# Kernel tuning notes

Hardware: AMD Instinct MI355X
Metric: run time of the kernel (lower is better)

The kernel has to match this reference:

```python
import jax, jax.numpy as jnp
import numpy as np

B, S, H = 2, 256, 768
LR = 0.01
EPS = 1e-5  # torch LayerNorm default


def setup_inputs() -> dict:
    key = jax.random.key(0)
    ks = jax.random.split(key, 6)
    f = jnp.float32
    return {
        "x": jax.random.normal(ks[0], (B, S, H), f),
        "W_init": jax.random.normal(ks[1], (H, H), f) * 0.02,
        "b_init": jnp.zeros((H,), f),
        "gate_w": jax.random.normal(ks[2], (4 * H, H), f) * 0.02,
        "gate_b": jnp.zeros((4 * H,), f),
        "up_w": jax.random.normal(ks[3], (4 * H, H), f) * 0.02,
        "up_b": jnp.zeros((4 * H,), f),
        "down_w": jax.random.normal(ks[4], (H, 4 * H), f) * 0.02,
        "down_b": jnp.zeros((H,), f),
        "norm_w": jnp.ones((H,), f),
        "norm_b": jnp.zeros((H,), f),
    }


def _layernorm(x, w, b):
    mu = jnp.mean(x, axis=-1, keepdims=True)
    var = jnp.var(x, axis=-1, keepdims=True)
    return (x - mu) * jax.lax.rsqrt(var + EPS) * w + b


def reference(x, W_init, b_init, gate_w, gate_b, up_w, up_b,
              down_w, down_b, norm_w, norm_b):
    # x: [B, S, H]. Sequential TTT fast-weight recurrence, vectorized over batch,
    # scanned over time (equivalent to the per-token Python loop in torch).
    Bn, Sn, Hn = x.shape
    xs = jnp.swapaxes(x, 0, 1)                                   # [S, B, H]
    x_next = jnp.concatenate([xs[1:], jnp.zeros_like(xs[:1])], 0)  # target x[t+1]
    # lr per step; the update is skipped at the last token (t == S-1)
    lr = jnp.concatenate([jnp.full((Sn - 1,), LR, x.dtype),
                          jnp.zeros((1,), x.dtype)])

    W0 = jnp.broadcast_to(W_init, (Bn, Hn, Hn))
    b0 = jnp.broadcast_to(b_init, (Bn, Hn))

    def step(carry, inp):
        W, b = carry
        xt, xn, lr_t = inp
        pred = jnp.einsum('bij,bj->bi', W, xt) + b               # fast-weight matvec
        gated = jax.nn.sigmoid(pred @ gate_w.T + gate_b) * (pred @ up_w.T + up_b)
        out = _layernorm(gated @ down_w.T + down_b + pred, norm_w, norm_b)
        diff = pred - xn                                         # prediction error
        W = W - lr_t * diff[:, :, None] * xt[:, None, :]         # rank-1 update
        b = b - lr_t * diff
        return (W, b), out

    _, ys = jax.lax.scan(step, (W0, b0), (xs, x_next, lr))       # ys: [S, B, H]
    return jnp.swapaxes(ys, 0, 1)
```

## Files before the change

kernel.cpp:

```cpp
#include <hip/hip_runtime.h>
#include <hip/hip_bf16.h>

#define H   768
#define H4  3072
#define S   256
#define BB  2
#define M   (BB * S)
#define LRC 0.01f
#define C   64
#define NC  (S / C)

typedef __attribute__((ext_vector_type(8))) short bf16x8;
typedef __attribute__((ext_vector_type(4))) float f32x4;

__device__ inline short bfbits(float f) {
    __hip_bfloat16 h = __float2bfloat16(f);
    return *reinterpret_cast<short*>(&h);
}

__global__ __launch_bounds__(256) void k_stage(
    const float* __restrict__ x,  const float* __restrict__ W0,
    const float* __restrict__ gw, const float* __restrict__ uw,
    const float* __restrict__ dw,
    short* __restrict__ Xhi, short* __restrict__ Xlo,
    short* __restrict__ Whi, short* __restrict__ Wlo,
    short* __restrict__ gw2, short* __restrict__ uw2, short* __restrict__ dw2)
{
    const long gid = (long)blockIdx.x * 256 + threadIdx.x;
    const float* src; short* hp; short* lp = nullptr; long base;
    if (gid < 98304)        { src = x;  hp = Xhi; lp = Xlo; base = 0; }
    else if (gid < 245760)  { src = W0; hp = Whi; lp = Wlo; base = 98304; }
    else if (gid < 835584)  { src = gw; hp = gw2; base = 245760; }
    else if (gid < 1425408) { src = uw; hp = uw2; base = 835584; }
    else                    { src = dw; hp = dw2; base = 1425408; }
    const long i = (gid - base) * 4;
    const float4 v = *(const float4*)(src + i);
    const float vf[4] = {v.x, v.y, v.z, v.w};
    short h4[4], l4[4];
#pragma unroll
    for (int j = 0; j < 4; ++j) {
        h4[j] = bfbits(vf[j]);
        __hip_bfloat16 hb = *reinterpret_cast<__hip_bfloat16*>(&h4[j]);
        l4[j] = bfbits(vf[j] - __bfloat162float(hb));
    }
    *(uint2*)(hp + i) = *(uint2*)h4;
    if (lp) *(uint2*)(lp + i) = *(uint2*)l4;
}

__global__ __launch_bounds__(256) void k_gram_base(
    const short* __restrict__ Xhi, const short* __restrict__ Xlo,
    const short* __restrict__ Whi, const short* __restrict__ Wlo,
    const float* __restrict__ b0,
    float* __restrict__ g, float* __restrict__ base0)
{
    const int wid = threadIdx.x >> 6, lane = threadIdx.x & 63;
    const int r16 = lane & 15, quad = lane >> 4;
    const int id = blockIdx.x;

    f32x4 acc[4];
#pragma unroll
    for (int i = 0; i < 4; ++i) acc[i] = (f32x4){0, 0, 0, 0};

    if (id < 32) {
        const int bx = id & 3, by = (id >> 2) & 3, b = id >> 4;
        const int m0 = by * 64, n0 = bx * 64 + wid * 16;
        const short* XH = Xhi + b * S * H;
        const short* XL = Xlo + b * S * H;
        for (int k0 = 0; k0 < H; k0 += 32) {
            const int k = k0 + quad * 8;
            const bf16x8 bh = *(const bf16x8*)(XH + (n0 + r16) * H + k);
            const bf16x8 bl = *(const bf16x8*)(XL + (n0 + r16) * H + k);
#pragma unroll
            for (int i = 0; i < 4; ++i) {
                const bf16x8 ah = *(const bf16x8*)(XH + (m0 + i * 16 + r16) * H + k);
                const bf16x8 al = *(const bf16x8*)(XL + (m0 + i * 16 + r16) * H + k);
                acc[i] = __builtin_amdgcn_mfma_f32_16x16x32_bf16(ah, bh, acc[i], 0, 0, 0);
                acc[i] = __builtin_amdgcn_mfma_f32_16x16x32_bf16(ah, bl, acc[i], 0, 0, 0);
                acc[i] = __builtin_amdgcn_mfma_f32_16x16x32_bf16(al, bh, acc[i], 0, 0, 0);
            }
        }
        const int col = n0 + r16;
#pragma unroll
        for (int i = 0; i < 4; ++i)
#pragma unroll
            for (int r = 0; r < 4; ++r) {
                const int row = m0 + i * 16 + quad * 4 + r;
                g[(b * S + row) * S + col] = acc[i][r] + 1.f;
            }
    } else {
        const int id2 = id - 32;
        const int m0 = (id2 / 12) * 64, n0 = (id2 % 12) * 64 + wid * 16;
        for (int k0 = 0; k0 < H; k0 += 32) {
            const int k = k0 + quad * 8;
            const bf16x8 bh = *(const bf16x8*)(Whi + (n0 + r16) * H + k);
            const bf16x8 bl = *(const bf16x8*)(Wlo + (n0 + r16) * H + k);
#pragma unroll
            for (int i = 0; i < 4; ++i) {
                const bf16x8 ah = *(const bf16x8*)(Xhi + (m0 + i * 16 + r16) * H + k);
                const bf16x8 al = *(const bf16x8*)(Xlo + (m0 + i * 16 + r16) * H + k);
                acc[i] = __builtin_amdgcn_mfma_f32_16x16x32_bf16(ah, bh, acc[i], 0, 0, 0);
                acc[i] = __builtin_amdgcn_mfma_f32_16x16x32_bf16(ah, bl, acc[i], 0, 0, 0);
                acc[i] = __builtin_amdgcn_mfma_f32_16x16x32_bf16(al, bh, acc[i], 0, 0, 0);
            }
        }
        const int col = n0 + r16;
        const float bv = b0[col];
#pragma unroll
        for (int i = 0; i < 4; ++i)
#pragma unroll
            for (int r = 0; r < 4; ++r) {
                const int row = m0 + i * 16 + quad * 4 + r;
                base0[row * H + col] = acc[i][r] + bv;
            }
    }
}

__global__ __launch_bounds__(256) void k_inv(
    const float* __restrict__ g, float* __restrict__ U)
{
    __shared__ float Gi[C * 65];
    const int tid = threadIdx.x;
    const int w = tid >> 6, lane = tid & 63;
    const int b = blockIdx.x >> 2, c = blockIdx.x & 3;
    const int t0 = c * C;

#pragma unroll
    for (int j = 0; j < 16; ++j) {
        const int idx = tid + 256 * j;
        const int row = idx >> 6, col = idx & 63;
        Gi[row * 65 + col] = g[(long)(b * S + t0 + row) * S + t0 + col];
    }
    __syncthreads();

    const int j0 = w * 16;
    float R[16];
#pragma unroll
    for (int i = 0; i < 16; ++i) R[i] = (lane == j0 + i) ? 1.f : 0.f;

    for (int s = 0; s < C - 1; ++s) {
        const float Gv = Gi[s * 65 + lane];
        const float mlt = (lane > s) ? LRC : 0.f;
#pragma unroll
        for (int i = 0; i < 16; ++i) {
            const float dsb = __shfl(R[i], s, 64);
            R[i] -= mlt * Gv * dsb;
        }
    }
    float* Ub = U + (long)(b * NC + c) * C * C;
#pragma unroll
    for (int i = 0; i < 16; ++i)
        Ub[lane * C + j0 + i] = R[i];
}

__global__ __launch_bounds__(256) void k_recur5(
    const float* __restrict__ x,
    const float* __restrict__ base0,
    const float* __restrict__ g,
    const float* __restrict__ U,
    float* __restrict__ pred_f,
    __hip_bfloat16* __restrict__ pred_h)
{
    __shared__ float tB[64 * 17];
    __shared__ float tX[64 * 17];
    __shared__ float Dl[256 * 17];
    __shared__ float Us[64 * 65];
    __shared__ float Gslab[192 * 64];
    const int tid = threadIdx.x;
    const int w = tid >> 6, lane = tid & 63;
    const int b = blockIdx.x / 48, hb = blockIdx.x % 48;
    const int h0 = hb * 16;
    const int ho = w * 4;
    const int ct = tid >> 2;
    const int cq = (tid & 3) * 4;

    for (int c = 0; c < NC; ++c) {
        const int t0 = c * C;
        __syncthreads();
        {
            const int gm = b * S + t0 + ct;
            const float4 bv = *(const float4*)(base0 + gm * H + h0 + cq);
            float4 xv = {0.f, 0.f, 0.f, 0.f};
            if (t0 + ct + 1 < S)
                xv = *(const float4*)(x + (gm + 1) * H + h0 + cq);
            tB[ct * 17 + cq + 0] = bv.x - xv.x;
            tB[ct * 17 + cq + 1] = bv.y - xv.y;
            tB[ct * 17 + cq + 2] = bv.z - xv.z;
            tB[ct * 17 + cq + 3] = bv.w - xv.w;
            tX[ct * 17 + cq + 0] = xv.x;
            tX[ct * 17 + cq + 1] = xv.y;
            tX[ct * 17 + cq + 2] = xv.z;
            tX[ct * 17 + cq + 3] = xv.w;
            const float* Ub = U + (long)(b * NC + c) * C * C;
#pragma unroll
            for (int j = 0; j < 16; ++j) {
                const int idx = tid + 256 * j;
                const int row = idx >> 6, col = idx & 63;
                Us[row * 65 + col] = Ub[row * C + col];
            }
            const float* gb = g + (long)(b * S) * S + t0;
            for (int i = tid; i < t0 * 64; i += 256) {
                const int row = i >> 6, col = i & 63;
                Gslab[i] = gb[(long)row * S + col];
            }
        }
        __syncthreads();
        float R[4], Xn[4];
#pragma unroll
        for (int h = 0; h < 4; ++h) {
            R[h]  = tB[lane * 17 + ho + h];
            Xn[h] = tX[lane * 17 + ho + h];
        }
#pragma unroll 4
        for (int cs = 0; cs < t0; ++cs) {
            const float Gv = Gslab[cs * 64 + lane];
            const float* dr = &Dl[cs * 17 + ho];
            R[0] -= LRC * Gv * dr[0];
            R[1] -= LRC * Gv * dr[1];
            R[2] -= LRC * Gv * dr[2];
            R[3] -= LRC * Gv * dr[3];
        }
        float D[4] = {0.f, 0.f, 0.f, 0.f};
#pragma unroll 8
        for (int s = 0; s < C; ++s) {
            const float Gv = Us[lane * 65 + s];
#pragma unroll
            for (int h = 0; h < 4; ++h) {
                const float dsb = __shfl(R[h], s, 64);
                D[h] += Gv * dsb;
            }
        }
#pragma unroll
        for (int h = 0; h < 4; ++h) Dl[(t0 + lane) * 17 + ho + h] = D[h];
        __syncthreads();
#pragma unroll
        for (int h = 0; h < 4; ++h) tB[lane * 17 + ho + h] = D[h] + Xn[h];
        __syncthreads();
        {
            const int gm = b * S + t0 + ct;
            float4 pv;
            pv.x = tB[ct * 17 + cq + 0];
            pv.y = tB[ct * 17 + cq + 1];
            pv.z = tB[ct * 17 + cq + 2];
            pv.w = tB[ct * 17 + cq + 3];
            *(float4*)(pred_f + gm * H + h0 + cq) = pv;
            short p4[4];
            p4[0] = bfbits(pv.x); p4[1] = bfbits(pv.y);
            p4[2] = bfbits(pv.z); p4[3] = bfbits(pv.w);
            *(uint2*)((short*)pred_h + gm * H + h0 + cq) = *(uint2*)p4;
        }
    }
}

#define RS 40
__global__ __launch_bounds__(256) void k_gateup3(
    const __hip_bfloat16* __restrict__ predh,
    const short* __restrict__ gwp, const float* __restrict__ gb,
    const short* __restrict__ uwp, const float* __restrict__ ub,
    __hip_bfloat16* __restrict__ hid)
{
    __shared__ int4 smv[1600];
    short* sm = (short*)smv;
    short* sA = sm;
    short* sG = sm + 64 * RS;
    short* sU = sm + (64 + 128) * RS;

    const int tid = threadIdx.x;
    const int wid = tid >> 6, lane = tid & 63;
    const int r16 = lane & 15, quad = lane >> 4;
    const int wm = wid & 1, wn = wid >> 1;
    const int n0 = blockIdx.x * 128;
    const int m0 = blockIdx.y * 64;

    const int srow = tid >> 2;
    const int sch  = (tid & 3) * 8;
    const short* A = (const short*)predh;

    f32x4 ag[2][4], au[2][4];
#pragma unroll
    for (int i = 0; i < 2; ++i)
#pragma unroll
        for (int j = 0; j < 4; ++j) { ag[i][j] = (f32x4){0,0,0,0}; au[i][j] = (f32x4){0,0,0,0}; }

    int4 rA, rG0, rG1, rU0, rU1;
    {
        const int k = sch;
        rA  = *(const int4*)(A   + (m0 + srow) * H + k);
        rG0 = *(const int4*)(gwp + (n0 + srow) * H + k);
        rG1 = *(const int4*)(gwp + (n0 + 64 + srow) * H + k);
        rU0 = *(const int4*)(uwp + (n0 + srow) * H + k);
        rU1 = *(const int4*)(uwp + (n0 + 64 + srow) * H + k);
    }
    for (int it = 0; it < 24; ++it) {
        *(int4*)(sA + srow * RS + sch)        = rA;
        *(int4*)(sG + srow * RS + sch)        = rG0;
        *(int4*)(sG + (64 + srow) * RS + sch) = rG1;
        *(int4*)(sU + srow * RS + sch)        = rU0;
        *(int4*)(sU + (64 + srow) * RS + sch) = rU1;
        __syncthreads();
        if (it < 23) {
            const int k = (it + 1) * 32 + sch;
            rA  = *(const int4*)(A   + (m0 + srow) * H + k);
            rG0 = *(const int4*)(gwp + (n0 + srow) * H + k);
            rG1 = *(const int4*)(gwp + (n0 + 64 + srow) * H + k);
            rU0 = *(const int4*)(uwp + (n0 + srow) * H + k);
            rU1 = *(const int4*)(uwp + (n0 + 64 + srow) * H + k);
        }
        bf16x8 aF[2], gF[4], uF[4];
#pragma unroll
        for (int i = 0; i < 2; ++i)
            aF[i] = *(const bf16x8*)(sA + (wm * 32 + i * 16 + r16) * RS + quad * 8);
#pragma unroll
        for (int j = 0; j < 4; ++j) {
            gF[j] = *(const bf16x8*)(sG + (wn * 64 + j * 16 + r16) * RS + quad * 8);
            uF[j] = *(const bf16x8*)(sU + (wn * 64 + j * 16 + r16) * RS + quad * 8);
        }
#pragma unroll
        for (int i = 0; i < 2; ++i)
#pragma unroll
            for (int j = 0; j < 4; ++j) {
                ag[i][j] = __builtin_amdgcn_mfma_f32_16x16x32_bf16(aF[i], gF[j], ag[i][j], 0, 0, 0);
                au[i][j] = __builtin_amdgcn_mfma_f32_16x16x32_bf16(aF[i], uF[j], au[i][j], 0, 0, 0);
            }
        __syncthreads();
    }
#pragma unroll
    for (int j = 0; j < 4; ++j) {
        const int ocol = n0 + wn * 64 + j * 16 + r16;
        const float gbv = gb[ocol], ubv = ub[ocol];
#pragma unroll
        for (int i = 0; i < 2; ++i)
#pragma unroll
            for (int r = 0; r < 4; ++r) {
                const int orow = m0 + wm * 32 + i * 16 + quad * 4 + r;
                const float gg = ag[i][j][r] + gbv;
                const float u  = au[i][j][r] + ubv;
                const float sg = 1.f / (1.f + __expf(-gg));
                hid[orow * H4 + ocol] = __float2bfloat16(sg * u);
            }
    }
}

__device__ inline bf16x8 ldb16(const void* p, long off) {
    return *(const bf16x8*)((const short*)p + off);
}
__global__ __launch_bounds__(256) void k_down2b(
    const __hip_bfloat16* __restrict__ hid,
    const short* __restrict__ dwp, const float* __restrict__ db,
    const float* __restrict__ predf, float* __restrict__ dout)
{
    const int wid = threadIdx.x >> 6, lane = threadIdx.x & 63;
    const int r16 = lane & 15, quad = lane >> 4;
    const int m0 = blockIdx.y * 32;
    const int n0 = blockIdx.x * 64 + wid * 16;

    f32x4 ac[2];
    ac[0] = (f32x4){0,0,0,0}; ac[1] = (f32x4){0,0,0,0};
    const short* A = (const short*)hid;
    const long brow = (long)(n0 + r16) * H4;

    for (int k0 = 0; k0 < H4; k0 += 32) {
        const int k = k0 + quad * 8;
        const bf16x8 bd = ldb16(dwp, brow + k);
#pragma unroll
        for (int i = 0; i < 2; ++i) {
            const bf16x8 af = *(const bf16x8*)(A + (m0 + i * 16 + r16) * H4 + k);
            ac[i] = __builtin_amdgcn_mfma_f32_16x16x32_bf16(af, bd, ac[i], 0, 0, 0);
        }
    }
    const int ocol = n0 + r16;
    const float dbv = db[ocol];
#pragma unroll
    for (int i = 0; i < 2; ++i)
#pragma unroll
        for (int r = 0; r < 4; ++r) {
            const int orow = m0 + i * 16 + quad * 4 + r;
            dout[orow * H + ocol] = ac[i][r] + dbv + predf[orow * H + ocol];
        }
}

__device__ inline bf16x8 ldb32(const void* p, long off) {
    const float* f = (const float*)p + off;
    const float4 a = *(const float4*)f;
    const float4 b = *(const float4*)(f + 4);
    bf16x8 r;
    r[0] = bfbits(a.x); r[1] = bfbits(a.y); r[2] = bfbits(a.z); r[3] = bfbits(a.w);
    r[4] = bfbits(b.x); r[5] = bfbits(b.y); r[6] = bfbits(b.z); r[7] = bfbits(b.w);
    return r;
}

__global__ __launch_bounds__(256) void k_gateup2(
    const __hip_bfloat16* __restrict__ predh,
    const void* __restrict__ gw, const float* __restrict__ gb,
    const void* __restrict__ uw, const float* __restrict__ ub,
    __hip_bfloat16* __restrict__ hid)
{
    const int wid = threadIdx.x >> 6, lane = threadIdx.x & 63;
    const int r16 = lane & 15, quad = lane >> 4;
    const int m0 = blockIdx.y * 64;
    const int n0 = blockIdx.x * 64 + wid * 16;

    f32x4 ag[4], au[4];
#pragma unroll
    for (int i = 0; i < 4; ++i) { ag[i] = (f32x4){0,0,0,0}; au[i] = (f32x4){0,0,0,0}; }
    const short* A = (const short*)predh;
    const long brow = (long)(n0 + r16) * H;

    for (int k0 = 0; k0 < H; k0 += 32) {
        const int k = k0 + quad * 8;
        const bf16x8 bg = ldb32(gw, brow + k);
        const bf16x8 bu = ldb32(uw, brow + k);
#pragma unroll
        for (int i = 0; i < 4; ++i) {
            const bf16x8 af = *(const bf16x8*)(A + (m0 + i * 16 + r16) * H + k);
            ag[i] = __builtin_amdgcn_mfma_f32_16x16x32_bf16(af, bg, ag[i], 0, 0, 0);
            au[i] = __builtin_amdgcn_mfma_f32_16x16x32_bf16(af, bu, au[i], 0, 0, 0);
        }
    }
    const int ocol = n0 + r16;
    const float gbv = gb[ocol], ubv = ub[ocol];
#pragma unroll
    for (int i = 0; i < 4; ++i)
#pragma unroll
        for (int r = 0; r < 4; ++r) {
            const int orow = m0 + i * 16 + quad * 4 + r;
            const float gg = ag[i][r] + gbv;
            const float u = au[i][r] + ubv;
            const float sg = 1.f / (1.f + __expf(-gg));
            hid[orow * H4 + ocol] = __float2bfloat16(sg * u);
        }
}

__global__ __launch_bounds__(256) void k_down2f(
    const __hip_bfloat16* __restrict__ hid,
    const void* __restrict__ dw, const float* __restrict__ db,
    const float* __restrict__ predf, float* __restrict__ dout)
{
    const int wid = threadIdx.x >> 6, lane = threadIdx.x & 63;
    const int r16 = lane & 15, quad = lane >> 4;
    const int m0 = blockIdx.y * 32;
    const int n0 = blockIdx.x * 64 + wid * 16;

    f32x4 ac[2];
    ac[0] = (f32x4){0,0,0,0}; ac[1] = (f32x4){0,0,0,0};
    const short* A = (const short*)hid;
    const long brow = (long)(n0 + r16) * H4;

    for (int k0 = 0; k0 < H4; k0 += 32) {
        const int k = k0 + quad * 8;
        const bf16x8 bd = ldb32(dw, brow + k);
#pragma unroll
        for (int i = 0; i < 2; ++i) {
            const bf16x8 af = *(const bf16x8*)(A + (m0 + i * 16 + r16) * H4 + k);
            ac[i] = __builtin_amdgcn_mfma_f32_16x16x32_bf16(af, bd, ac[i], 0, 0, 0);
        }
    }
    const int ocol = n0 + r16;
    const float dbv = db[ocol];
#pragma unroll
    for (int i = 0; i < 2; ++i)
#pragma unroll
        for (int r = 0; r < 4; ++r) {
            const int orow = m0 + i * 16 + quad * 4 + r;
            dout[orow * H + ocol] = ac[i][r] + dbv + predf[orow * H + ocol];
        }
}

__global__ __launch_bounds__(256) void k_ln(
    const float* __restrict__ dout,
    const float* __restrict__ nw,
    const float* __restrict__ nb,
    float* __restrict__ out)
{
    const int m = blockIdx.x;
    const int tid = threadIdx.x;
    const float* rowp = dout + m * H;

    float v[3];
    float s = 0.f, s2 = 0.f;
#pragma unroll
    for (int j = 0; j < 3; ++j) {
        v[j] = rowp[tid + 256 * j];
        s += v[j];
        s2 += v[j] * v[j];
    }
#pragma unroll
    for (int off = 32; off >= 1; off >>= 1) {
        s  += __shfl_xor(s, off, 64);
        s2 += __shfl_xor(s2, off, 64);
    }
    __shared__ float rs[4], rs2[4];
    const int wid = tid >> 6, lane = tid & 63;
    if (lane == 0) { rs[wid] = s; rs2[wid] = s2; }
    __syncthreads();
    s  = rs[0] + rs[1] + rs[2] + rs[3];
    s2 = rs2[0] + rs2[1] + rs2[2] + rs2[3];
    const float mu  = s / (float)H;
    const float var = s2 / (float)H - mu * mu;
    const float inv = rsqrtf(var + 1e-5f);
#pragma unroll
    for (int j = 0; j < 3; ++j) {
        const int hh = tid + 256 * j;
        out[m * H + hh] = (v[j] - mu) * inv * nw[hh] + nb[hh];
    }
}

extern "C" void kernel_launch(void* const* d_in, const int* in_sizes, int n_in,
                              void* d_out, int out_size, void* d_ws, size_t ws_size,
                              hipStream_t stream)
{
    const float* x   = (const float*)d_in[0];
    const float* W0  = (const float*)d_in[1];
    const float* b0  = (const float*)d_in[2];
    const float* gw  = (const float*)d_in[3];
    const float* gb  = (const float*)d_in[4];
    const float* uw  = (const float*)d_in[5];
    const float* ub  = (const float*)d_in[6];
    const float* dw  = (const float*)d_in[7];
    const float* db  = (const float*)d_in[8];
    const float* nw  = (const float*)d_in[9];
    const float* nb  = (const float*)d_in[10];

    char* ws = (char*)d_ws;
    float*          pred_f = (float*)(ws);
    __hip_bfloat16* pred_h = (__hip_bfloat16*)(ws + 1572864);
    __hip_bfloat16* hid    = (__hip_bfloat16*)(ws + 2359296);
    float*          base0  = (float*)(ws + 5505024);
    float*          dout_f = (float*)(ws + 5505024);
    float*          g      = (float*)(ws + 7077888);
    short*          Xhi    = (short*)(ws + 7602176);
    short*          Xlo    = (short*)(ws + 8388608);
    short*          Whi    = (short*)(ws + 9175040);
    short*          Wlo    = (short*)(ws + 10354688);
    float*          U      = (float*)(ws + 11534336);
    const size_t WNEED = 11665408ULL + 3ULL * 4718592ULL;
    const bool wb = ws_size >= WNEED;
    short* gw2 = (short*)(ws + 11665408);
    short* uw2 = (short*)(ws + 11665408 + 4718592);
    short* dw2 = (short*)(ws + 11665408 + 2 * 4718592);

    const int ngroups = wb ? 2015232 : 245760;
    k_stage<<<dim3(ngroups / 256), 256, 0, stream>>>(
        x, W0, gw, uw, dw, Xhi, Xlo, Whi, Wlo, gw2, uw2, dw2);
    k_gram_base<<<dim3(128), 256, 0, stream>>>(Xhi, Xlo, Whi, Wlo, b0, g, base0);
    k_inv<<<dim3(BB * NC), 256, 0, stream>>>(g, U);
    k_recur5<<<dim3(96), 256, 0, stream>>>(x, base0, g, U, pred_f, pred_h);
    if (wb) {
        k_gateup3<<<dim3(H4 / 128, M / 64), 256, 0, stream>>>(pred_h, gw2, gb, uw2, ub, hid);
        k_down2b<<<dim3(H / 64, M / 32), 256, 0, stream>>>(hid, dw2, db, pred_f, dout_f);
    } else {
        k_gateup2<<<dim3(H4 / 64, M / 64), 256, 0, stream>>>(pred_h, gw, gb, uw, ub, hid);
        k_down2f<<<dim3(H / 64, M / 32), 256, 0, stream>>>(hid, dw, db, pred_f, dout_f);
    }
    k_ln<<<dim3(M), 256, 0, stream>>>(dout_f, nw, nb, (float*)d_out);
}
```

Measured before the change: 223.2 us.

## Split-K down projection, smaller gate/up tiles, LDS broadcast in recurrence

```diff
diff --git a/kernel.cpp b/kernel.cpp
--- a/kernel.cpp
+++ b/kernel.cpp
@@ -152,7 +152,7 @@
         Ub[lane * C + j0 + i] = R[i];
 }
 
-__global__ __launch_bounds__(256) void k_recur5(
+__global__ __launch_bounds__(256) void k_recur6(
     const float* __restrict__ x,
     const float* __restrict__ base0,
     const float* __restrict__ g,
@@ -160,11 +160,12 @@
     float* __restrict__ pred_f,
     __hip_bfloat16* __restrict__ pred_h)
 {
-    __shared__ float tB[64 * 17];
-    __shared__ float tX[64 * 17];
-    __shared__ float Dl[256 * 17];
-    __shared__ float Us[64 * 65];
-    __shared__ float Gslab[192 * 64];
+    __shared__ float  tB[64 * 17];
+    __shared__ float  tX[64 * 17];
+    __shared__ float4 Dl4[256 * 4];
+    __shared__ float4 Rl4[4 * 64];
+    __shared__ float  Us[64 * 65];
+    __shared__ float  Gslab[192 * 64];
     const int tid = threadIdx.x;
     const int w = tid >> 6, lane = tid & 63;
     const int b = blockIdx.x / 48, hb = blockIdx.x % 48;
@@ -213,24 +214,24 @@
 #pragma unroll 4
         for (int cs = 0; cs < t0; ++cs) {
             const float Gv = Gslab[cs * 64 + lane];
-            const float* dr = &Dl[cs * 17 + ho];
-            R[0] -= LRC * Gv * dr[0];
-            R[1] -= LRC * Gv * dr[1];
-            R[2] -= LRC * Gv * dr[2];
-            R[3] -= LRC * Gv * dr[3];
-        }
+            const float4 dr = Dl4[cs * 4 + w];
+            R[0] -= LRC * Gv * dr.x;
+            R[1] -= LRC * Gv * dr.y;
+            R[2] -= LRC * Gv * dr.z;
+            R[3] -= LRC * Gv * dr.w;
+        }
+        Rl4[w * 64 + lane] = (float4){R[0], R[1], R[2], R[3]};
         float D[4] = {0.f, 0.f, 0.f, 0.f};
 #pragma unroll 8
         for (int s = 0; s < C; ++s) {
-            const float Gv = Us[lane * 65 + s];
-#pragma unroll
-            for (int h = 0; h < 4; ++h) {
-                const float dsb = __shfl(R[h], s, 64);
-                D[h] += Gv * dsb;
-            }
-        }
-#pragma unroll
-        for (int h = 0; h < 4; ++h) Dl[(t0 + lane) * 17 + ho + h] = D[h];
+            const float4 rb = Rl4[w * 64 + s];
+            const float uv = Us[lane * 65 + s];
+            D[0] += uv * rb.x;
+            D[1] += uv * rb.y;
+            D[2] += uv * rb.z;
+            D[3] += uv * rb.w;
+        }
+        Dl4[(t0 + lane) * 4 + w] = (float4){D[0], D[1], D[2], D[3]};
         __syncthreads();
 #pragma unroll
         for (int h = 0; h < 4; ++h) tB[lane * 17 + ho + h] = D[h] + Xn[h];
@@ -252,80 +253,69 @@
 }
 
 #define RS 40
-__global__ __launch_bounds__(256) void k_gateup3(
+__global__ __launch_bounds__(256) void k_gateup4(
     const __hip_bfloat16* __restrict__ predh,
     const short* __restrict__ gwp, const float* __restrict__ gb,
     const short* __restrict__ uwp, const float* __restrict__ ub,
     __hip_bfloat16* __restrict__ hid)
 {
-    __shared__ int4 smv[1600];
+    __shared__ int4 smv[960];
     short* sm = (short*)smv;
     short* sA = sm;
     short* sG = sm + 64 * RS;
-    short* sU = sm + (64 + 128) * RS;
+    short* sU = sm + 128 * RS;
 
     const int tid = threadIdx.x;
     const int wid = tid >> 6, lane = tid & 63;
     const int r16 = lane & 15, quad = lane >> 4;
-    const int wm = wid & 1, wn = wid >> 1;
-    const int n0 = blockIdx.x * 128;
+    const int wm = wid & 1, wn = (wid >> 1) & 1;
+    const int n0 = blockIdx.x * 64;
     const int m0 = blockIdx.y * 64;
 
     const int srow = tid >> 2;
     const int sch  = (tid & 3) * 8;
     const short* A = (const short*)predh;
 
-    f32x4 ag[2][4], au[2][4];
+    f32x4 ag[2][2], au[2][2];
 #pragma unroll
     for (int i = 0; i < 2; ++i)
 #pragma unroll
-        for (int j = 0; j < 4; ++j) { ag[i][j] = (f32x4){0,0,0,0}; au[i][j] = (f32x4){0,0,0,0}; }
-
-    int4 rA, rG0, rG1, rU0, rU1;
-    {
-        const int k = sch;
-        rA  = *(const int4*)(A   + (m0 + srow) * H + k);
-        rG0 = *(const int4*)(gwp + (n0 + srow) * H + k);
-        rG1 = *(const int4*)(gwp + (n0 + 64 + srow) * H + k);
-        rU0 = *(const int4*)(uwp + (n0 + srow) * H + k);
-        rU1 = *(const int4*)(uwp + (n0 + 64 + srow) * H + k);
-    }
+        for (int j = 0; j < 2; ++j) { ag[i][j] = (f32x4){0,0,0,0}; au[i][j] = (f32x4){0,0,0,0}; }
+
+    int4 rA, rG, rU;
+    rA = *(const int4*)(A   + (m0 + srow) * H + sch);
+    rG = *(const int4*)(gwp + (n0 + srow) * H + sch);
+    rU = *(const int4*)(uwp + (n0 + srow) * H + sch);
     for (int it = 0; it < 24; ++it) {
-        *(int4*)(sA + srow * RS + sch)        = rA;
-        *(int4*)(sG + srow * RS + sch)        = rG0;
-        *(int4*)(sG + (64 + srow) * RS + sch) = rG1;
-        *(int4*)(sU + srow * RS + sch)        = rU0;
-        *(int4*)(sU + (64 + srow) * RS + sch) = rU1;
+        *(int4*)(sA + srow * RS + sch) = rA;
+        *(int4*)(sG + srow * RS + sch) = rG;
+        *(int4*)(sU + srow * RS + sch) = rU;
         __syncthreads();
         if (it < 23) {
             const int k = (it + 1) * 32 + sch;
-            rA  = *(const int4*)(A   + (m0 + srow) * H + k);
-            rG0 = *(const int4*)(gwp + (n0 + srow) * H + k);
-            rG1 = *(const int4*)(gwp + (n0 + 64 + srow) * H + k);
-            rU0 = *(const int4*)(uwp + (n0 + srow) * H + k);
-            rU1 = *(const int4*)(uwp + (n0 + 64 + srow) * H + k);
-        }
-        bf16x8 aF[2], gF[4], uF[4];
+            rA = *(const int4*)(A   + (m0 + srow) * H + k);
+            rG = *(const int4*)(gwp + (n0 + srow) * H + k);
+            rU = *(const int4*)(uwp + (n0 + srow) * H + k);
+        }
+        bf16x8 aF[2], gF[2], uF[2];
+#pragma unroll
+        for (int i = 0; i < 2; ++i) {
+            aF[i] = *(const bf16x8*)(sA + (wm * 32 + i * 16 + r16) * RS + quad * 8);
+            gF[i] = *(const bf16x8*)(sG + (wn * 32 + i * 16 + r16) * RS + quad * 8);
+            uF[i] = *(const bf16x8*)(sU + (wn * 32 + i * 16 + r16) * RS + quad * 8);
+        }
 #pragma unroll
         for (int i = 0; i < 2; ++i)
-            aF[i] = *(const bf16x8*)(sA + (wm * 32 + i * 16 + r16) * RS + quad * 8);
-#pragma unroll
-        for (int j = 0; j < 4; ++j) {
-            gF[j] = *(const bf16x8*)(sG + (wn * 64 + j * 16 + r16) * RS + quad * 8);
-            uF[j] = *(const bf16x8*)(sU + (wn * 64 + j * 16 + r16) * RS + quad * 8);
-        }
-#pragma unroll
-        for (int i = 0; i < 2; ++i)
-#pragma unroll
-            for (int j = 0; j < 4; ++j) {
+#pragma unroll
+            for (int j = 0; j < 2; ++j) {
                 ag[i][j] = __builtin_amdgcn_mfma_f32_16x16x32_bf16(aF[i], gF[j], ag[i][j], 0, 0, 0);
                 au[i][j] = __builtin_amdgcn_mfma_f32_16x16x32_bf16(aF[i], uF[j], au[i][j], 0, 0, 0);
             }
         __syncthreads();
     }
 #pragma unroll
-    for (int j = 0; j < 4; ++j) {
-        const int ocol = n0 + wn * 64 + j * 16 + r16;
+    for (int j = 0; j < 2; ++j) {
+        const int ocol = n0 + wn * 32 + j * 16 + r16;
         const float gbv = gb[ocol], ubv = ub[ocol];
 #pragma unroll
         for (int i = 0; i < 2; ++i)
@@ -343,22 +333,24 @@
 __device__ inline bf16x8 ldb16(const void* p, long off) {
     return *(const bf16x8*)((const short*)p + off);
 }
-__global__ __launch_bounds__(256) void k_down2b(
+__global__ __launch_bounds__(256) void k_down4(
     const __hip_bfloat16* __restrict__ hid,
-    const short* __restrict__ dwp, const float* __restrict__ db,
-    const float* __restrict__ predf, float* __restrict__ dout)
+    const short* __restrict__ dwp,
+    float* __restrict__ dpart)
 {
     const int wid = threadIdx.x >> 6, lane = threadIdx.x & 63;
     const int r16 = lane & 15, quad = lane >> 4;
     const int m0 = blockIdx.y * 32;
     const int n0 = blockIdx.x * 64 + wid * 16;
+    const int kz = blockIdx.z;
 
     f32x4 ac[2];
     ac[0] = (f32x4){0,0,0,0}; ac[1] = (f32x4){0,0,0,0};
     const short* A = (const short*)hid;
     const long brow = (long)(n0 + r16) * H4;
 
-    for (int k0 = 0; k0 < H4; k0 += 32) {
+    const int kbeg = kz * 768, kend = kbeg + 768;
+    for (int k0 = kbeg; k0 < kend; k0 += 32) {
         const int k = k0 + quad * 8;
         const bf16x8 bd = ldb16(dwp, brow + k);
 #pragma unroll
@@ -367,15 +359,60 @@
             ac[i] = __builtin_amdgcn_mfma_f32_16x16x32_bf16(af, bd, ac[i], 0, 0, 0);
         }
     }
+    float* dp = dpart + (long)kz * M * H;
     const int ocol = n0 + r16;
-    const float dbv = db[ocol];
 #pragma unroll
     for (int i = 0; i < 2; ++i)
 #pragma unroll
         for (int r = 0; r < 4; ++r) {
             const int orow = m0 + i * 16 + quad * 4 + r;
-            dout[orow * H + ocol] = ac[i][r] + dbv + predf[orow * H + ocol];
-        }
+            dp[orow * H + ocol] = ac[i][r];
+        }
+}
+
+__global__ __launch_bounds__(256) void k_ln2(
+    const float* __restrict__ dpart,
+    const float* __restrict__ db,
+    const float* __restrict__ predf,
+    const float* __restrict__ nw,
+    const float* __restrict__ nb,
+    float* __restrict__ out)
+{
+    const int m = blockIdx.x;
+    const int tid = threadIdx.x;
+
+    float v[3];
+    float s = 0.f, s2 = 0.f;
+#pragma unroll
+    for (int j = 0; j < 3; ++j) {
+        const int hh = tid + 256 * j;
+        const long o = (long)m * H + hh;
+        float t = dpart[o] + dpart[o + (long)M * H]
+                + dpart[o + 2L * M * H] + dpart[o + 3L * M * H]
+                + db[hh] + predf[o];
+        v[j] = t;
+        s += t;
+        s2 += t * t;
+    }
+#pragma unroll
+    for (int off = 32; off >= 1; off >>= 1) {
+        s  += __shfl_xor(s, off, 64);
+        s2 += __shfl_xor(s2, off, 64);
+    }
+    __shared__ float rs[4], rs2[4];
+    const int wid = tid >> 6, lane = tid & 63;
+    if (lane == 0) { rs[wid] = s; rs2[wid] = s2; }
+    __syncthreads();
+    s  = rs[0] + rs[1] + rs[2] + rs[3];
+    s2 = rs2[0] + rs2[1] + rs2[2] + rs2[3];
+    const float mu  = s / (float)H;
+    const float var = s2 / (float)H - mu * mu;
+    const float inv = rsqrtf(var + 1e-5f);
+#pragma unroll
+    for (int j = 0; j < 3; ++j) {
+        const int hh = tid + 256 * j;
+        out[m * H + hh] = (v[j] - mu) * inv * nw[hh] + nb[hh];
+    }
 }
 
 __device__ inline bf16x8 ldb32(const void* p, long off) {
@@ -465,7 +502,7 @@
         }
 }
 
-__global__ __launch_bounds__(256) void k_ln(
+__global__ __launch_bounds__(256) void k_ln1(
     const float* __restrict__ dout,
     const float* __restrict__ nw,
     const float* __restrict__ nb,
@@ -532,24 +569,26 @@
     short*          Whi    = (short*)(ws + 9175040);
     short*          Wlo    = (short*)(ws + 10354688);
     float*          U      = (float*)(ws + 11534336);
-    const size_t WNEED = 11665408ULL + 3ULL * 4718592ULL;
-    const bool wb = ws_size >= WNEED;
     short* gw2 = (short*)(ws + 11665408);
     short* uw2 = (short*)(ws + 11665408 + 4718592);
     short* dw2 = (short*)(ws + 11665408 + 2 * 4718592);
+    float* dpart = (float*)(ws + 25821184);
+    const size_t WNEED = 25821184ULL + 6291456ULL;
+    const bool wb = ws_size >= WNEED;
 
     const int ngroups = wb ? 2015232 : 245760;
     k_stage<<<dim3(ngroups / 256), 256, 0, stream>>>(
         x, W0, gw, uw, dw, Xhi, Xlo, Whi, Wlo, gw2, uw2, dw2);
     k_gram_base<<<dim3(128), 256, 0, stream>>>(Xhi, Xlo, Whi, Wlo, b0, g, base0);
     k_inv<<<dim3(BB * NC), 256, 0, stream>>>(g, U);
-    k_recur5<<<dim3(96), 256, 0, stream>>>(x, base0, g, U, pred_f, pred_h);
+    k_recur6<<<dim3(96), 256, 0, stream>>>(x, base0, g, U, pred_f, pred_h);
     if (wb) {
-        k_gateup3<<<dim3(H4 / 128, M / 64), 256, 0, stream>>>(pred_h, gw2, gb, uw2, ub, hid);
-        k_down2b<<<dim3(H / 64, M / 32), 256, 0, stream>>>(hid, dw2, db, pred_f, dout_f);
+        k_gateup4<<<dim3(H4 / 64, M / 64), 256, 0, stream>>>(pred_h, gw2, gb, uw2, ub, hid);
+        k_down4<<<dim3(H / 64, M / 32, 4), 256, 0, stream>>>(hid, dw2, dpart);
+        k_ln2<<<dim3(M), 256, 0, stream>>>(dpart, db, pred_f, nw, nb, (float*)d_out);
     } else {
         k_gateup2<<<dim3(H4 / 64, M / 64), 256, 0, stream>>>(pred_h, gw, gb, uw, ub, hid);
         k_down2f<<<dim3(H / 64, M / 32), 256, 0, stream>>>(hid, dw, db, pred_f, dout_f);
-    }
-    k_ln<<<dim3(M), 256, 0, stream>>>(dout_f, nw, nb, (float*)d_out);
-}
+        k_ln1<<<dim3(M), 256, 0, stream>>>(dout_f, nw, nb, (float*)d_out);
+    }
+}
```

After: 205.8 us. -7.8%, faster.
